# Optimization experiments

Measured on AMD Instinct MI355X. Metric: run time of the kernel, lower is better.

## Reference

```python
import jax, jax.numpy as jnp
import numpy as np

B, W, N, DIM, GAMMA = 32, 16, 256, 256, 4
WH = 16  # sqrt(N)
V = DIM // GAMMA
TABLE = (2 * WH - 1) * (2 * WH - 1)  # 961


def _make_rel_index(wh: int) -> np.ndarray:
    coords = np.stack(np.meshgrid(np.arange(wh), np.arange(wh), indexing='ij'))  # (2, wh, wh)
    flat = coords.reshape(2, -1)                         # (2, wh*wh)
    rel = flat[:, :, None] - flat[:, None, :]            # (2, n, n)
    rel = rel.transpose(1, 2, 0).copy()                  # (n, n, 2)
    rel[:, :, 0] += wh - 1
    rel[:, :, 1] += wh - 1
    rel[:, :, 0] *= 2 * wh - 1
    return rel.sum(-1).astype(np.int32)                  # (n, n)


def setup_inputs() -> dict:
    key = jax.random.key(0)
    k1, k2, k3 = jax.random.split(key, 3)
    x = jax.random.normal(k1, (B, W, N, DIM), dtype=jnp.float32)
    bias_table = jax.random.normal(k2, (TABLE, W * GAMMA), dtype=jnp.float32) * 0.02
    token_bias = jax.random.normal(k3, (W * GAMMA, N, 1), dtype=jnp.float32) * 0.02
    rel_index = jnp.asarray(_make_rel_index(WH))
    return {"x": x, "bias_table": bias_table, "token_bias": token_bias, "rel_index": rel_index}


def reference(x, bias_table, token_bias, rel_index):
    b, w, n, d = x.shape
    gamma = GAMMA
    v = d // gamma
    # gather: (n, n, w*gamma) -> permute to (w*gamma, n, n)
    rpb = bias_table[rel_index.reshape(-1)].reshape(n, n, w * gamma)
    rpb = jnp.transpose(rpb, (2, 0, 1))                  # ((s w), n, n) with s outer
    # rearrange '(s b) m n -> b m n s'
    win_weight = jnp.transpose(rpb.reshape(gamma, w, n, n), (1, 2, 3, 0))  # (w, m, n, s)
    # rearrange 'b w n (v s) -> b w n v s'
    xs = x.reshape(b, w, n, v, gamma)
    out = jnp.einsum('wmns,bwnvs->bwmvs', win_weight, xs)
    # rearrange '(w s) m v -> w m v s'
    bias = jnp.transpose(token_bias.reshape(w, gamma, n, 1), (0, 2, 3, 1))  # (w, m, 1, s)
    out = out + bias[None]
    return out.reshape(b, w, n, d)
```

## Files before the change

### kernel.cpp

```cpp
#include <hip/hip_runtime.h>
#include <stdint.h>


typedef __attribute__((ext_vector_type(8))) short bf16x8;
typedef __attribute__((ext_vector_type(4))) float f32x4;
typedef __attribute__((ext_vector_type(8))) unsigned short u16x8;

__device__ __forceinline__ unsigned short f2bf(float f) {
    union { float f; unsigned u; } v; v.f = f;
    unsigned u = v.u;
    u += 0x7FFFu + ((u >> 16) & 1u);
    return (unsigned short)(u >> 16);
}
__device__ __forceinline__ float bf2f(unsigned short h) {
    union { unsigned u; float f; } v; v.u = ((unsigned)h) << 16;
    return v.f;
}
__device__ __forceinline__ int expInRange(unsigned short w16) {
    int e = (w16 >> 7) & 0xFF;
    return (e >= 100 && e <= 140) ? 1 : 0;
}

__global__ __launch_bounds__(256) void k_gather(
    const void* __restrict__ bt_raw,
    const int*  __restrict__ rel_index,
    const void* __restrict__ x_raw,
    unsigned short* __restrict__ Ab)
{
    const unsigned short* xw = (const unsigned short*)x_raw;
    int t = threadIdx.x;
    int pred = expInRange(xw[t * 2]) & expInRange(xw[t * 2 + 1]);
    int cnt = __syncthreads_count(pred);
    bool isF32 = (cnt < 150);

    int idx4 = blockIdx.x * 256 + t;
    int base = idx4 << 2;
    int nn = base & 255;
    int m  = (base >> 8) & 255;
    int ws = base >> 16;
    int colw = ((ws & 3) << 4) + (ws >> 2);
    const int* ri = rel_index + (m << 8) + nn;
    int i0 = ri[0], i1 = ri[1], i2 = ri[2], i3 = ri[3];
    ushort4 o;
    if (isF32) {
        const float* bt = (const float*)bt_raw;
        o.x = f2bf(bt[(i0 << 6) + colw]);
        o.y = f2bf(bt[(i1 << 6) + colw]);
        o.z = f2bf(bt[(i2 << 6) + colw]);
        o.w = f2bf(bt[(i3 << 6) + colw]);
    } else {
        const unsigned short* bt = (const unsigned short*)bt_raw;
        o.x = bt[(i0 << 6) + colw];
        o.y = bt[(i1 << 6) + colw];
        o.z = bt[(i2 << 6) + colw];
        o.w = bt[(i3 << 6) + colw];
    }
    *(ushort4*)(Ab + base) = o;
}

__global__ __launch_bounds__(512, 4) void k_main(
    const void* __restrict__ x_raw,
    const unsigned short* __restrict__ Ab,
    const void* __restrict__ tb_raw,
    void* __restrict__ out_raw)
{
    __shared__ unsigned short lds[16384 + 8192];

    const int tid  = threadIdx.x;
    const unsigned short* xw = (const unsigned short*)x_raw;
    int pred = expInRange(xw[tid]);
    int cnt = __syncthreads_count(pred);
    const bool isF32 = (cnt < 400);

    const int lane = tid & 63;
    const int wave = tid >> 6;
    const int bx = blockIdx.x;
    const int b  = bx & 31;
    const int mt = (bx >> 5) & 1;
    const int w  = bx >> 6;
    const int m0 = mt << 7;

    const int sw   = wave & 3;
    const int vh   = wave >> 2;
    const int vvb  = vh << 5;
    const int col  = lane & 15;
    const int quad = lane >> 4;

    const int a_row = tid >> 2;
    const int a_nn8 = (tid & 3) << 3;
    unsigned short* AsW = lds + (a_row << 5) + a_nn8;
    const unsigned short* Ag = Ab + (w << 18) + ((m0 + a_row) << 8) + a_nn8;

    const int x_nn = tid & 31;
    const int x_vg = tid >> 5;
    const int xoff = (((b << 4) + w) << 16) + (x_nn << 8) + (x_vg << 4);
    const float*          Xgf = (const float*)x_raw + xoff;
    const unsigned short* Xgh = (const unsigned short*)x_raw + xoff;
    unsigned short* XsW = lds + 16384 + x_nn;

    f32x4 acc[8][2];
#pragma unroll
    for (int mi = 0; mi < 8; mi++) {
        acc[mi][0] = (f32x4){0.f, 0.f, 0.f, 0.f};
        acc[mi][1] = (f32x4){0.f, 0.f, 0.f, 0.f};
    }

    const unsigned short* AsR = lds + (sw << 12) + (col << 5) + (quad << 3);
    const unsigned short* XsR = lds + 16384 + (sw << 11) + ((vvb + col) << 5) + (quad << 3);

    for (int nc = 0; nc < 8; nc++) {
        u16x8 av[4];
#pragma unroll
        for (int it = 0; it < 4; it++)
            av[it] = *(const u16x8*)(Ag + (it << 16) + (nc << 5));
#pragma unroll
        for (int it = 0; it < 4; it++)
            *(u16x8*)(AsW + (it << 12)) = av[it];

        if (isF32) {
            float4 v[4];
#pragma unroll
            for (int i = 0; i < 4; i++)
                v[i] = *(const float4*)(Xgf + (nc << 13) + (i << 2));
            const float* vf = (const float*)v;
#pragma unroll
            for (int j = 0; j < 16; j++) {
                int vv = (x_vg << 2) + (j >> 2);
                XsW[((j & 3) << 11) + (vv << 5)] = f2bf(vf[j]);
            }
        } else {
            u16x8 xv0 = *(const u16x8*)(Xgh + (nc << 13));
            u16x8 xv1 = *(const u16x8*)(Xgh + (nc << 13) + 8);
#pragma unroll
            for (int j = 0; j < 8; j++) {
                int vv = (x_vg << 2) + (j >> 2);
                XsW[((j & 3) << 11) + (vv << 5)] = xv0[j];
            }
#pragma unroll
            for (int j = 0; j < 8; j++) {
                int vv = (x_vg << 2) + 2 + (j >> 2);
                XsW[((j & 3) << 11) + (vv << 5)] = xv1[j];
            }
        }
        __syncthreads();

        bf16x8 bfr0 = *(const bf16x8*)(XsR);
        bf16x8 bfr1 = *(const bf16x8*)(XsR + 512);
#pragma unroll
        for (int mi = 0; mi < 8; mi++) {
            bf16x8 afr = *(const bf16x8*)(AsR + (mi << 9));
            acc[mi][0] = __builtin_amdgcn_mfma_f32_16x16x32_bf16(afr, bfr0, acc[mi][0], 0, 0, 0);
            acc[mi][1] = __builtin_amdgcn_mfma_f32_16x16x32_bf16(afr, bfr1, acc[mi][1], 0, 0, 0);
        }
        __syncthreads();
    }

    const int tboff = (((w << 2) + sw) << 8) + m0;
    const int ooff  = (((b << 4) + w) << 16) + (m0 << 8) + sw;
    if (isF32) {
        const float* tb = (const float*)tb_raw + tboff;
        float* ob = (float*)out_raw + ooff;
#pragma unroll
        for (int mi = 0; mi < 8; mi++) {
#pragma unroll
            for (int r = 0; r < 4; r++) {
                int m = (mi << 4) + (quad << 2) + r;
                float bias = tb[m];
#pragma unroll
                for (int vi = 0; vi < 2; vi++) {
                    int vv = vvb + (vi << 4) + col;
                    ob[(m << 8) + (vv << 2)] = acc[mi][vi][r] + bias;
                }
            }
        }
    } else {
        const unsigned short* tb = (const unsigned short*)tb_raw + tboff;
        unsigned short* ob = (unsigned short*)out_raw + ooff;
#pragma unroll
        for (int mi = 0; mi < 8; mi++) {
#pragma unroll
            for (int r = 0; r < 4; r++) {
                int m = (mi << 4) + (quad << 2) + r;
                float bias = bf2f(tb[m]);
#pragma unroll
                for (int vi = 0; vi < 2; vi++) {
                    int vv = vvb + (vi << 4) + col;
                    ob[(m << 8) + (vv << 2)] = f2bf(acc[mi][vi][r] + bias);
                }
            }
        }
    }
}

__global__ __launch_bounds__(512, 4) void k_main_fused(
    const void* __restrict__ x_raw,
    const void* __restrict__ bt_raw,
    const int*  __restrict__ rel_index,
    const void* __restrict__ tb_raw,
    void* __restrict__ out_raw)
{
    __shared__ unsigned short lds[16384 + 8192];

    const int tid  = threadIdx.x;
    const unsigned short* xw = (const unsigned short*)x_raw;
    int pred = expInRange(xw[tid]);
    int cnt = __syncthreads_count(pred);
    const bool isF32 = (cnt < 400);

    const int lane = tid & 63;
    const int wave = tid >> 6;
    const int bx = blockIdx.x;
    const int b  = bx & 31;
    const int mt = (bx >> 5) & 1;
    const int w  = bx >> 6;
    const int m0 = mt << 7;

    const int sw   = wave & 3;
    const int vh   = wave >> 2;
    const int vvb  = vh << 5;
    const int col  = lane & 15;
    const int quad = lane >> 4;

    const int a_row = tid >> 2;
    const int a_nn8 = (tid & 3) << 3;
    unsigned short* AsW = lds + (a_row << 5) + a_nn8;
    const int* rIp = rel_index + ((m0 + a_row) << 8) + a_nn8;

    const int x_nn = tid & 31;
    const int x_vg = tid >> 5;
    const int xoff = (((b << 4) + w) << 16) + (x_nn << 8) + (x_vg << 4);
    const float*          Xgf = (const float*)x_raw + xoff;
    const unsigned short* Xgh = (const unsigned short*)x_raw + xoff;
    unsigned short* XsW = lds + 16384 + x_nn;

    f32x4 acc[8][2];
#pragma unroll
    for (int mi = 0; mi < 8; mi++) {
        acc[mi][0] = (f32x4){0.f, 0.f, 0.f, 0.f};
        acc[mi][1] = (f32x4){0.f, 0.f, 0.f, 0.f};
    }

    const unsigned short* AsR = lds + (sw << 12) + (col << 5) + (quad << 3);
    const unsigned short* XsR = lds + 16384 + (sw << 11) + ((vvb + col) << 5) + (quad << 3);

    for (int nc = 0; nc < 8; nc++) {
        int4 r0 = *(const int4*)(rIp + (nc << 5));
        int4 r1 = *(const int4*)(rIp + (nc << 5) + 4);
        int ri[8] = {r0.x, r0.y, r0.z, r0.w, r1.x, r1.y, r1.z, r1.w};
#pragma unroll
        for (int it = 0; it < 4; it++) {
            u16x8 av;
            if (isF32) {
                const float* bt = (const float*)bt_raw;
#pragma unroll
                for (int j = 0; j < 8; j++)
                    av[j] = f2bf(bt[(ri[j] << 6) + (it << 4) + w]);
            } else {
                const unsigned short* bt = (const unsigned short*)bt_raw;
#pragma unroll
                for (int j = 0; j < 8; j++)
                    av[j] = bt[(ri[j] << 6) + (it << 4) + w];
            }
            *(u16x8*)(AsW + (it << 12)) = av;
        }

        if (isF32) {
            float4 v[4];
#pragma unroll
            for (int i = 0; i < 4; i++)
                v[i] = *(const float4*)(Xgf + (nc << 13) + (i << 2));
            const float* vf = (const float*)v;
#pragma unroll
            for (int j = 0; j < 16; j++) {
                int vv = (x_vg << 2) + (j >> 2);
                XsW[((j & 3) << 11) + (vv << 5)] = f2bf(vf[j]);
            }
        } else {
            u16x8 xv0 = *(const u16x8*)(Xgh + (nc << 13));
            u16x8 xv1 = *(const u16x8*)(Xgh + (nc << 13) + 8);
#pragma unroll
            for (int j = 0; j < 8; j++) {
                int vv = (x_vg << 2) + (j >> 2);
                XsW[((j & 3) << 11) + (vv << 5)] = xv0[j];
            }
#pragma unroll
            for (int j = 0; j < 8; j++) {
                int vv = (x_vg << 2) + 2 + (j >> 2);
                XsW[((j & 3) << 11) + (vv << 5)] = xv1[j];
            }
        }
        __syncthreads();

        bf16x8 bfr0 = *(const bf16x8*)(XsR);
        bf16x8 bfr1 = *(const bf16x8*)(XsR + 512);
#pragma unroll
        for (int mi = 0; mi < 8; mi++) {
            bf16x8 afr = *(const bf16x8*)(AsR + (mi << 9));
            acc[mi][0] = __builtin_amdgcn_mfma_f32_16x16x32_bf16(afr, bfr0, acc[mi][0], 0, 0, 0);
            acc[mi][1] = __builtin_amdgcn_mfma_f32_16x16x32_bf16(afr, bfr1, acc[mi][1], 0, 0, 0);
        }
        __syncthreads();
    }

    const int tboff = (((w << 2) + sw) << 8) + m0;
    const int ooff  = (((b << 4) + w) << 16) + (m0 << 8) + sw;
    if (isF32) {
        const float* tb = (const float*)tb_raw + tboff;
        float* ob = (float*)out_raw + ooff;
#pragma unroll
        for (int mi = 0; mi < 8; mi++) {
#pragma unroll
            for (int r = 0; r < 4; r++) {
                int m = (mi << 4) + (quad << 2) + r;
                float bias = tb[m];
#pragma unroll
                for (int vi = 0; vi < 2; vi++) {
                    int vv = vvb + (vi << 4) + col;
                    ob[(m << 8) + (vv << 2)] = acc[mi][vi][r] + bias;
                }
            }
        }
    } else {
        const unsigned short* tb = (const unsigned short*)tb_raw + tboff;
        unsigned short* ob = (unsigned short*)out_raw + ooff;
#pragma unroll
        for (int mi = 0; mi < 8; mi++) {
#pragma unroll
            for (int r = 0; r < 4; r++) {
                int m = (mi << 4) + (quad << 2) + r;
                float bias = bf2f(tb[m]);
#pragma unroll
                for (int vi = 0; vi < 2; vi++) {
                    int vv = vvb + (vi << 4) + col;
                    ob[(m << 8) + (vv << 2)] = f2bf(acc[mi][vi][r] + bias);
                }
            }
        }
    }
}

extern "C" void kernel_launch(void* const* d_in, const int* in_sizes, int n_in,
                              void* d_out, int out_size, void* d_ws, size_t ws_size,
                              hipStream_t stream) {
    const void* x          = d_in[0];
    const void* bias_table = d_in[1];
    const void* token_bias = d_in[2];
    const int*  rel_index  = (const int*)d_in[3];

    const size_t AB_BYTES = (size_t)64 * 256 * 256 * 2;
    if (ws_size >= AB_BYTES) {
        unsigned short* Ab = (unsigned short*)d_ws;
        hipLaunchKernelGGL(k_gather, dim3(4096), dim3(256), 0, stream,
                           bias_table, rel_index, x, Ab);
        hipLaunchKernelGGL(k_main, dim3(1024), dim3(512), 0, stream,
                           x, Ab, token_bias, d_out);
    } else {
        hipLaunchKernelGGL(k_main_fused, dim3(1024), dim3(512), 0, stream,
                           x, bias_table, rel_index, token_bias, d_out);
    }
}
```

Baseline: 290.9 us.

## Double-buffer k_main with direct global-to-LDS loads and smaller M tiles

Restructures k_main to use double-buffered LDS, loading the gathered bias matrix straight into LDS via global_load_lds. X is register-prefetched two chunks ahead, and its LDS layout is swizzled to reduce bank conflicts. The M tile is halved to 64 rows so the grid doubles to 2048 blocks. The gather kernel now writes 8 elements per thread with vectorized index loads. The aim is to overlap memory with MFMA and remove one barrier per iteration, at the cost of halving A reuse per block and re-reading X twice as often.

```diff
diff --git a/kernel.cpp b/kernel.cpp
--- a/kernel.cpp
+++ b/kernel.cpp
@@ -20,6 +20,10 @@
     int e = (w16 >> 7) & 0xFF;
     return (e >= 100 && e <= 140) ? 1 : 0;
 }
+
+#define GLL16(gp, lp) __builtin_amdgcn_global_load_lds( \
+    (const __attribute__((address_space(1))) void*)(gp), \
+    (__attribute__((address_space(3))) void*)(lp), 16, 0, 0)
 
 __global__ __launch_bounds__(256) void k_gather(
     const void* __restrict__ bt_raw,
@@ -33,29 +37,27 @@
     int cnt = __syncthreads_count(pred);
     bool isF32 = (cnt < 150);
 
-    int idx4 = blockIdx.x * 256 + t;
-    int base = idx4 << 2;
+    int idx8 = blockIdx.x * 256 + t;
+    int base = idx8 << 3;
     int nn = base & 255;
     int m  = (base >> 8) & 255;
     int ws = base >> 16;
     int colw = ((ws & 3) << 4) + (ws >> 2);
     const int* ri = rel_index + (m << 8) + nn;
-    int i0 = ri[0], i1 = ri[1], i2 = ri[2], i3 = ri[3];
-    ushort4 o;
+    int4 r0 = *(const int4*)ri;
+    int4 r1 = *(const int4*)(ri + 4);
+    int idx[8] = {r0.x, r0.y, r0.z, r0.w, r1.x, r1.y, r1.z, r1.w};
+    u16x8 o;
     if (isF32) {
         const float* bt = (const float*)bt_raw;
-        o.x = f2bf(bt[(i0 << 6) + colw]);
-        o.y = f2bf(bt[(i1 << 6) + colw]);
-        o.z = f2bf(bt[(i2 << 6) + colw]);
-        o.w = f2bf(bt[(i3 << 6) + colw]);
+#pragma unroll
+        for (int j = 0; j < 8; j++) o[j] = f2bf(bt[(idx[j] << 6) + colw]);
     } else {
         const unsigned short* bt = (const unsigned short*)bt_raw;
-        o.x = bt[(i0 << 6) + colw];
-        o.y = bt[(i1 << 6) + colw];
-        o.z = bt[(i2 << 6) + colw];
-        o.w = bt[(i3 << 6) + colw];
-    }
-    *(ushort4*)(Ab + base) = o;
+#pragma unroll
+        for (int j = 0; j < 8; j++) o[j] = bt[(idx[j] << 6) + colw];
+    }
+    *(u16x8*)(Ab + base) = o;
 }
 
 __global__ __launch_bounds__(512, 4) void k_main(
@@ -64,7 +66,7 @@
     const void* __restrict__ tb_raw,
     void* __restrict__ out_raw)
 {
-    __shared__ unsigned short lds[16384 + 8192];
+    __shared__ unsigned short lds[32768];
 
     const int tid  = threadIdx.x;
     const unsigned short* xw = (const unsigned short*)x_raw;
@@ -76,9 +78,9 @@
     const int wave = tid >> 6;
     const int bx = blockIdx.x;
     const int b  = bx & 31;
-    const int mt = (bx >> 5) & 1;
-    const int w  = bx >> 6;
-    const int m0 = mt << 7;
+    const int mt = (bx >> 5) & 3;
+    const int w  = bx >> 7;
+    const int m0 = mt << 6;
 
     const int sw   = wave & 3;
     const int vh   = wave >> 2;
@@ -86,73 +88,90 @@
     const int col  = lane & 15;
     const int quad = lane >> 4;
 
-    const int a_row = tid >> 2;
-    const int a_nn8 = (tid & 3) << 3;
-    unsigned short* AsW = lds + (a_row << 5) + a_nn8;
-    const unsigned short* Ag = Ab + (w << 18) + ((m0 + a_row) << 8) + a_nn8;
-
-    const int x_nn = tid & 31;
-    const int x_vg = tid >> 5;
-    const int xoff = (((b << 4) + w) << 16) + (x_nn << 8) + (x_vg << 4);
-    const float*          Xgf = (const float*)x_raw + xoff;
-    const unsigned short* Xgh = (const unsigned short*)x_raw + xoff;
-    unsigned short* XsW = lds + 16384 + x_nn;
-
-    f32x4 acc[8][2];
-#pragma unroll
-    for (int mi = 0; mi < 8; mi++) {
+    const int g1 = 512 + tid;
+    const unsigned short* Ag0 = Ab + (((w << 2) + (tid >> 8)) << 16) + ((m0 + ((tid >> 2) & 63)) << 8) + ((tid & 3) << 3);
+    const unsigned short* Ag1 = Ab + (((w << 2) + (g1  >> 8)) << 16) + ((m0 + ((g1  >> 2) & 63)) << 8) + ((g1  & 3) << 3);
+
+    const int d0   = (tid & 127) << 1;
+    const int ngrp = tid >> 7;
+    const int xgoff = (((b << 4) + w) << 16) + (ngrp << 11) + d0;
+    const float*          Xgf = (const float*)x_raw + xgoff;
+    const unsigned short* Xgh = (const unsigned short*)x_raw + xgoff;
+    const int vvx   = d0 >> 2;
+    const int slotx = (ngrp ^ ((vvx >> 1) & 3)) << 3;
+    const int xw0 = 16384 + ((d0 & 3) << 11) + (vvx << 5) + slotx;
+    const int xw1 = xw0 + 2048;
+
+    const int vr0 = vvb + col;
+    const int sl0 = (quad ^ ((vr0 >> 1) & 3)) << 3;
+    const int xr0_off = 16384 + (sw << 11) + (vr0 << 5) + sl0;
+    const int xr1_off = xr0_off + (16 << 5);
+    const int ar = (sw << 11) + (col << 5) + (quad << 3);
+
+    f32x4 acc[4][2];
+#pragma unroll
+    for (int mi = 0; mi < 4; mi++) {
         acc[mi][0] = (f32x4){0.f, 0.f, 0.f, 0.f};
         acc[mi][1] = (f32x4){0.f, 0.f, 0.f, 0.f};
     }
 
-    const unsigned short* AsR = lds + (sw << 12) + (col << 5) + (quad << 3);
-    const unsigned short* XsR = lds + 16384 + (sw << 11) + ((vvb + col) << 5) + (quad << 3);
-
-    for (int nc = 0; nc < 8; nc++) {
-        u16x8 av[4];
-#pragma unroll
-        for (int it = 0; it < 4; it++)
-            av[it] = *(const u16x8*)(Ag + (it << 16) + (nc << 5));
-#pragma unroll
-        for (int it = 0; it < 4; it++)
-            *(u16x8*)(AsW + (it << 12)) = av[it];
-
+    float2       xrf[8];
+    unsigned int xru[8];
+
+    auto xpref = [&](int nc_) {
         if (isF32) {
-            float4 v[4];
-#pragma unroll
-            for (int i = 0; i < 4; i++)
-                v[i] = *(const float4*)(Xgf + (nc << 13) + (i << 2));
-            const float* vf = (const float*)v;
-#pragma unroll
-            for (int j = 0; j < 16; j++) {
-                int vv = (x_vg << 2) + (j >> 2);
-                XsW[((j & 3) << 11) + (vv << 5)] = f2bf(vf[j]);
-            }
+#pragma unroll
+            for (int j = 0; j < 8; j++)
+                xrf[j] = *(const float2*)(Xgf + (nc_ << 13) + (j << 8));
         } else {
-            u16x8 xv0 = *(const u16x8*)(Xgh + (nc << 13));
-            u16x8 xv1 = *(const u16x8*)(Xgh + (nc << 13) + 8);
-#pragma unroll
-            for (int j = 0; j < 8; j++) {
-                int vv = (x_vg << 2) + (j >> 2);
-                XsW[((j & 3) << 11) + (vv << 5)] = xv0[j];
-            }
-#pragma unroll
-            for (int j = 0; j < 8; j++) {
-                int vv = (x_vg << 2) + 2 + (j >> 2);
-                XsW[((j & 3) << 11) + (vv << 5)] = xv1[j];
-            }
-        }
-        __syncthreads();
-
-        bf16x8 bfr0 = *(const bf16x8*)(XsR);
-        bf16x8 bfr1 = *(const bf16x8*)(XsR + 512);
-#pragma unroll
-        for (int mi = 0; mi < 8; mi++) {
-            bf16x8 afr = *(const bf16x8*)(AsR + (mi << 9));
+#pragma unroll
+            for (int j = 0; j < 8; j++)
+                xru[j] = *(const unsigned int*)(Xgh + (nc_ << 13) + (j << 8));
+        }
+    };
+    auto xwrite = [&](int xb) {
+        u16x8 o0, o1;
+        if (isF32) {
+#pragma unroll
+            for (int j = 0; j < 8; j++) { o0[j] = f2bf(xrf[j].x); o1[j] = f2bf(xrf[j].y); }
+        } else {
+#pragma unroll
+            for (int j = 0; j < 8; j++) { o0[j] = (unsigned short)(xru[j] & 0xFFFFu);
+                                          o1[j] = (unsigned short)(xru[j] >> 16); }
+        }
+        *(u16x8*)(lds + xw0 + xb) = o0;
+        *(u16x8*)(lds + xw1 + xb) = o1;
+    };
+    auto agll = [&](int nc_, int ab) {
+        GLL16(Ag0 + (nc_ << 5), lds + ab + (wave << 9));
+        GLL16(Ag1 + (nc_ << 5), lds + ab + 4096 + (wave << 9));
+    };
+
+    agll(0, 0);
+    xpref(0);
+    xwrite(0);
+    xpref(1);
+    __syncthreads();
+
+#pragma unroll
+    for (int nc = 0; nc < 8; ++nc) {
+        const int cur = (nc & 1) << 13;
+        const int nxt = ((nc + 1) & 1) << 13;
+        if (nc < 7) {
+            agll(nc + 1, nxt);
+            xwrite(nxt);
+        }
+        if (nc < 6) xpref(nc + 2);
+
+        bf16x8 bfr0 = *(const bf16x8*)(lds + xr0_off + cur);
+        bf16x8 bfr1 = *(const bf16x8*)(lds + xr1_off + cur);
+#pragma unroll
+        for (int mi = 0; mi < 4; mi++) {
+            bf16x8 afr = *(const bf16x8*)(lds + cur + ar + (mi << 9));
             acc[mi][0] = __builtin_amdgcn_mfma_f32_16x16x32_bf16(afr, bfr0, acc[mi][0], 0, 0, 0);
             acc[mi][1] = __builtin_amdgcn_mfma_f32_16x16x32_bf16(afr, bfr1, acc[mi][1], 0, 0, 0);
         }
-        __syncthreads();
+        if (nc < 7) __syncthreads();
     }
 
     const int tboff = (((w << 2) + sw) << 8) + m0;
@@ -161,7 +180,7 @@
         const float* tb = (const float*)tb_raw + tboff;
         float* ob = (float*)out_raw + ooff;
 #pragma unroll
-        for (int mi = 0; mi < 8; mi++) {
+        for (int mi = 0; mi < 4; mi++) {
 #pragma unroll
             for (int r = 0; r < 4; r++) {
                 int m = (mi << 4) + (quad << 2) + r;
@@ -177,7 +196,7 @@
         const unsigned short* tb = (const unsigned short*)tb_raw + tboff;
         unsigned short* ob = (unsigned short*)out_raw + ooff;
 #pragma unroll
-        for (int mi = 0; mi < 8; mi++) {
+        for (int mi = 0; mi < 4; mi++) {
 #pragma unroll
             for (int r = 0; r < 4; r++) {
                 int m = (mi << 4) + (quad << 2) + r;
@@ -350,9 +369,9 @@
     const size_t AB_BYTES = (size_t)64 * 256 * 256 * 2;
     if (ws_size >= AB_BYTES) {
         unsigned short* Ab = (unsigned short*)d_ws;
-        hipLaunchKernelGGL(k_gather, dim3(4096), dim3(256), 0, stream,
+        hipLaunchKernelGGL(k_gather, dim3(2048), dim3(256), 0, stream,
                            bias_table, rel_index, x, Ab);
-        hipLaunchKernelGGL(k_main, dim3(1024), dim3(512), 0, stream,
+        hipLaunchKernelGGL(k_main, dim3(2048), dim3(512), 0, stream,
                            x, Ab, token_bias, d_out);
     } else {
         hipLaunchKernelGGL(k_main_fused, dim3(1024), dim3(512), 0, stream,
```

Measured after the change: 318.6 us. 9.5% more time.
